# Performance work log

Hardware: AMD Instinct MI355X
Metric: run time of the kernel (lower is better)

Reference implementation:

```python
import jax, jax.numpy as jnp
import numpy as np

D_MODEL = 512
N_HEADS = 8
D_KEYS = D_MODEL // N_HEADS  # 64
DIN = D_MODEL * 2            # 1024
DPROJ = D_KEYS * N_HEADS * 2 # 1024
B, L = 2, 2048


def setup_inputs() -> dict:
    key = jax.random.key(0)
    ks = jax.random.split(key, 11)
    s_in = 1.0 / np.sqrt(DIN)
    s_out = 1.0 / np.sqrt(DPROJ)
    return {
        "queries": jax.random.normal(ks[0], (B, L, DIN), jnp.float32),
        "keys": jax.random.normal(ks[1], (B, L, DIN), jnp.float32),
        "values": jax.random.normal(ks[2], (B, L, DIN), jnp.float32),
        "Wq": jax.random.normal(ks[3], (DPROJ, DIN), jnp.float32) * s_in,
        "bq": jax.random.normal(ks[4], (DPROJ,), jnp.float32) * s_in,
        "Wk": jax.random.normal(ks[5], (DPROJ, DIN), jnp.float32) * s_in,
        "bk": jax.random.normal(ks[6], (DPROJ,), jnp.float32) * s_in,
        "Wv": jax.random.normal(ks[7], (DPROJ, DIN), jnp.float32) * s_in,
        "bv": jax.random.normal(ks[8], (DPROJ,), jnp.float32) * s_in,
        "Wo": jax.random.normal(ks[9], (DIN, DPROJ), jnp.float32) * s_out,
        "bo": jax.random.normal(ks[10], (DIN,), jnp.float32) * s_out,
    }


def reference(queries, keys, values, Wq, bq, Wk, bk, Wv, bv, Wo, bo):
    b, l, _ = queries.shape
    H, E = N_HEADS, 2
    # projections: (B, L, DIN) -> (B, L, d_keys, H, 2)
    q = (queries @ Wq.T + bq).reshape(b, l, -1, H, E)
    k = (keys @ Wk.T + bk).reshape(b, l, -1, H, E)
    v = (values @ Wv.T + bv).reshape(b, l, -1, H, E)
    scale = 1.0 / np.sqrt(E)  # E=2 (real/imag)
    # attention over the d_keys axis, per token n, per head h
    scores = jnp.einsum('bnlhe,bnshe->bnhls', q, k)  # (B, L, H, dk, dk)
    A = jax.nn.softmax(scale * scores, axis=-1)
    out = jnp.einsum('bnhls,bnshd->bnlhd', A, v)     # (B, L, dk, H, 2)
    out = out.reshape(b, l, -1)                      # (B, L, dk*H*2)
    return out @ Wo.T + bo                           # (B, L, 2*d_model)
```

## Files before the change

### kernel.cpp

```cpp
#include <hip/hip_runtime.h>
#include <hip/hip_bf16.h>
#include <stdint.h>

#define TOK   4096
#define KDIM  1024
#define NDIM  1024
#define NHEAD 8

typedef _Float16 f16;
typedef __attribute__((ext_vector_type(2))) _Float16 h2;
typedef __attribute__((ext_vector_type(8))) _Float16 f16x8;
typedef __attribute__((ext_vector_type(4))) float f32x4;
typedef __attribute__((ext_vector_type(4))) uint u32x4;

__device__ __forceinline__ void gload_lds16(const void* g, void* l) {
    __builtin_amdgcn_global_load_lds(
        (const __attribute__((address_space(1))) void*)g,
        (__attribute__((address_space(3))) void*)l, 16, 0, 0);
}


struct CvtArgs {
    const float* src[7];
    void*        dst[7];
    int          n4[7];
    int          type[7];
};

__global__ __launch_bounds__(256) void cvt_kernel(CvtArgs a) {
    const int seg = blockIdx.y;
    const int type = a.type[seg];
    const float4* s = (const float4*)a.src[seg];
    const int n4 = a.n4[seg];
    const int stride = gridDim.x * blockDim.x;
    for (int i = blockIdx.x * blockDim.x + threadIdx.x; i < n4; i += stride) {
        float4 v = s[i];
        if (type == 0) {
            f16* d = (f16*)a.dst[seg];
            union { f16 h[4]; uint2 u; } o;
            o.h[0] = (f16)v.x; o.h[1] = (f16)v.y; o.h[2] = (f16)v.z; o.h[3] = (f16)v.w;
            *(uint2*)(d + (size_t)i * 4) = o.u;
        } else if (type == 1) {
            f16* d = (f16*)a.dst[seg];
            const int r = i >> 8, c = (i & 255) * 4;
            const int rp = ((r >> 1) & 7) * 128 + (r >> 4) * 2 + (r & 1);
            union { f16 h[4]; uint2 u; } o;
            o.h[0] = (f16)v.x; o.h[1] = (f16)v.y; o.h[2] = (f16)v.z; o.h[3] = (f16)v.w;
            *(uint2*)(d + (size_t)rp * 1024 + c) = o.u;
        } else {
            f16* d = (f16*)a.dst[seg];
            const int r = i >> 8, c = (i & 255) * 4;
            const int p0 = ((c >> 1) & 7) * 128 + (c >> 4) * 2;
            const int p1 = (((c + 2) >> 1) & 7) * 128 + ((c + 2) >> 4) * 2;
            union { f16 h[2]; uint u; } u01, u23;
            u01.h[0] = (f16)v.x; u01.h[1] = (f16)v.y;
            u23.h[0] = (f16)v.z; u23.h[1] = (f16)v.w;
            *(uint*)(d + (size_t)r * 1024 + p0) = u01.u;
            *(uint*)(d + (size_t)r * 1024 + p1) = u23.u;
        }
    }
}

struct GemmArgs {
    const f16*   A[3];
    const f16*   B[3];
    const float* bias[3];
    void*        C[3];
};

#define VM_WAIT6 asm volatile("s_waitcnt vmcnt(6)" ::: "memory")
#define VM_WAIT0 asm volatile("s_waitcnt vmcnt(0)" ::: "memory")

template<int OUTMODE>
__global__ __launch_bounds__(256) void gemm_bt_kernel(GemmArgs ga) {
    constexpr int K = KDIM, N = NDIM;
    constexpr int NT = K / 64;
    const f16*   A    = ga.A[blockIdx.z];
    const f16*   B    = ga.B[blockIdx.z];
    const float* bias = ga.bias[blockIdx.z];

    __shared__ f16 sm[2 * (128 * 64 + 64 * 64)];

    const int tid  = threadIdx.x;
    const int wave = tid >> 6, lane = tid & 63;
    const int wm = wave >> 1, wn = wave & 1;
    const int bm = blockIdx.x * 128, bn = blockIdx.y * 64;
    const int lrow = lane & 15, kgrp = lane >> 4;

    f32x4 acc[4][2] = {};

    const int colL = (lane & 7) << 3;
    const int colG = (((lane & 7) ^ ((lane >> 3) & 7)) << 3);
    const int arow = wave * 32 + (lane >> 3);
    const int brow = wave * 16 + (lane >> 3);

    auto stage = [&](int buf, int kt) {
        f16* As = sm + buf * (128 * 64 + 64 * 64);
        f16* Bs = As + 128 * 64;
        #pragma unroll
        for (int i = 0; i < 4; ++i) {
            const int row = arow + i * 8;
            gload_lds16(A + (size_t)(bm + row) * K + kt + colG, As + row * 64 + colL);
        }
        #pragma unroll
        for (int i = 0; i < 2; ++i) {
            const int row = brow + i * 8;
            gload_lds16(B + (size_t)(bn + row) * K + kt + colG, Bs + row * 64 + colL);
        }
    };

    stage(0, 0);

    const int swz = (lrow & 7) << 3;

    for (int it = 0; it < NT; ++it) {
        const int cur = it & 1;
        if (it + 1 < NT) {
            stage(cur ^ 1, (it + 1) * 64);
            VM_WAIT6;
        } else {
            VM_WAIT0;
        }
        __builtin_amdgcn_s_barrier();
        __builtin_amdgcn_sched_barrier(0);

        const f16* As = sm + cur * (128 * 64 + 64 * 64);
        const f16* Bs = As + 128 * 64;
        #pragma unroll
        for (int kk = 0; kk < 2; ++kk) {
            f16x8 af[4], bf[2];
            const int kcol = (kk * 32 + kgrp * 8) ^ swz;
            #pragma unroll
            for (int mi = 0; mi < 4; ++mi)
                af[mi] = *(const f16x8*)(As + (wm * 64 + mi * 16 + lrow) * 64 + kcol);
            #pragma unroll
            for (int ni = 0; ni < 2; ++ni)
                bf[ni] = *(const f16x8*)(Bs + (wn * 32 + ni * 16 + lrow) * 64 + kcol);
            #pragma unroll
            for (int mi = 0; mi < 4; ++mi)
                #pragma unroll
                for (int ni = 0; ni < 2; ++ni)
                    acc[mi][ni] = __builtin_amdgcn_mfma_f32_16x16x32_f16(af[mi], bf[ni], acc[mi][ni], 0, 0, 0);
        }
        __builtin_amdgcn_s_barrier();
    }

    const int rbase = kgrp * 4;
    #pragma unroll
    for (int mi = 0; mi < 4; ++mi) {
        #pragma unroll
        for (int ni = 0; ni < 2; ++ni) {
            const int col = bn + wn * 32 + ni * 16 + lrow;
            const int bidx = (OUTMODE == 0)
                ? (((col >> 1) & 63) * 16 + (col >> 7) * 2 + (col & 1))
                : col;
            const float bv = bias[bidx];
            #pragma unroll
            for (int r = 0; r < 4; ++r) {
                const int row = bm + wm * 64 + mi * 16 + rbase + r;
                const float v = acc[mi][ni][r] + bv;
                if constexpr (OUTMODE == 0)
                    ((f16*)ga.C[blockIdx.z])[(size_t)row * N + col] = (f16)v;
                else
                    ((float*)ga.C[blockIdx.z])[(size_t)row * N + col] = v;
            }
        }
    }
}

__global__ __launch_bounds__(256) void attn_kernel(const f16* qp, const f16* kp,
                                                   const f16* vp, f16* ao) {
    const int tid = threadIdx.x, wave = tid >> 6, lane = tid & 63;
    const int task = blockIdx.x * 4 + wave;
    const size_t base = (size_t)task * 64;
    const float SCALE = 0.70710678118f * 1.44269504089f;

    union U2 { uint u; h2 h; f16 s[2]; };
    U2 qu; qu.u = ((const uint*)qp)[base + lane];
    const float q0 = (float)qu.s[0] * SCALE, q1 = (float)qu.s[1] * SCALE;
#if __has_builtin(__builtin_amdgcn_fdot2)
    h2 qs; qs[0] = (f16)q0; qs[1] = (f16)q1;
#endif

    const u32x4* kb = (const u32x4*)((const uint*)kp + base);
    const u32x4* vb = (const u32x4*)((const uint*)vp + base);

    float sum = 0.f, o0 = 0.f, o1 = 0.f;
    #pragma unroll
    for (int g = 0; g < 4; ++g) {
        u32x4 kr[4], vr[4];
        #pragma unroll
        for (int i = 0; i < 4; ++i) { kr[i] = kb[g * 4 + i]; vr[i] = vb[g * 4 + i]; }
        #pragma unroll
        for (int i = 0; i < 4; ++i) {
            #pragma unroll
            for (int j = 0; j < 4; ++j) {
                U2 ku, vu;
                ku.u = kr[i][j];
                vu.u = vr[i][j];
#if __has_builtin(__builtin_amdgcn_fdot2)
                const float sc = __builtin_amdgcn_fdot2(qs, ku.h, 0.0f, false);
#else
                const float sc = fmaf(q0, (float)ku.s[0], q1 * (float)ku.s[1]);
#endif
#if __has_builtin(__builtin_amdgcn_exp2f)
                const float p = __builtin_amdgcn_exp2f(sc);
#else
                const float p = exp2f(sc);
#endif
                sum += p;
                o0 = fmaf(p, (float)vu.s[0], o0);
                o1 = fmaf(p, (float)vu.s[1], o1);
            }
        }
    }
    const float inv = __builtin_amdgcn_rcpf(sum);
    U2 o;
    o.s[0] = (f16)(o0 * inv);
    o.s[1] = (f16)(o1 * inv);
    ((uint*)ao)[base + lane] = o.u;
}

extern "C" void kernel_launch(void* const* d_in, const int* in_sizes, int n_in,
                              void* d_out, int out_size, void* d_ws, size_t ws_size,
                              hipStream_t stream) {
    const float* queries = (const float*)d_in[0];
    const float* keys    = (const float*)d_in[1];
    const float* values  = (const float*)d_in[2];
    const float* Wq = (const float*)d_in[3];
    const float* bq = (const float*)d_in[4];
    const float* Wk = (const float*)d_in[5];
    const float* bk = (const float*)d_in[6];
    const float* Wv = (const float*)d_in[7];
    const float* bv = (const float*)d_in[8];
    const float* Wo = (const float*)d_in[9];
    const float* bo = (const float*)d_in[10];

    char* ws = (char*)d_ws;
    const size_t MB = 1024 * 1024;
    f16* Xq  = (f16*)(ws + 0 * MB);
    f16* Xk  = (f16*)(ws + 8 * MB);
    f16* Xv  = (f16*)(ws + 16 * MB);
    f16* Wqh = (f16*)(ws + 24 * MB);
    f16* Wkh = (f16*)(ws + 26 * MB);
    f16* Wvh = (f16*)(ws + 28 * MB);
    f16* Woh = (f16*)(ws + 30 * MB);
    f16* qp  = (f16*)(ws + 32 * MB);
    f16* kp  = (f16*)(ws + 40 * MB);
    f16* vp  = (f16*)(ws + 48 * MB);
    f16* ao  = (f16*)(ws + 56 * MB);

    CvtArgs ca;
    ca.src[0] = queries; ca.dst[0] = Xq;  ca.n4[0] = TOK * KDIM / 4;  ca.type[0] = 0;
    ca.src[1] = keys;    ca.dst[1] = Xk;  ca.n4[1] = TOK * KDIM / 4;  ca.type[1] = 0;
    ca.src[2] = values;  ca.dst[2] = Xv;  ca.n4[2] = TOK * KDIM / 4;  ca.type[2] = 0;
    ca.src[3] = Wq;      ca.dst[3] = Wqh; ca.n4[3] = NDIM * KDIM / 4; ca.type[3] = 1;
    ca.src[4] = Wk;      ca.dst[4] = Wkh; ca.n4[4] = NDIM * KDIM / 4; ca.type[4] = 1;
    ca.src[5] = Wv;      ca.dst[5] = Wvh; ca.n4[5] = NDIM * KDIM / 4; ca.type[5] = 1;
    ca.src[6] = Wo;      ca.dst[6] = Woh; ca.n4[6] = NDIM * KDIM / 4; ca.type[6] = 2;
    cvt_kernel<<<dim3(256, 7), 256, 0, stream>>>(ca);

    GemmArgs g1;
    g1.A[0] = Xq;  g1.A[1] = Xk;  g1.A[2] = Xv;
    g1.B[0] = Wqh; g1.B[1] = Wkh; g1.B[2] = Wvh;
    g1.bias[0] = bq; g1.bias[1] = bk; g1.bias[2] = bv;
    g1.C[0] = qp; g1.C[1] = kp; g1.C[2] = vp;
    gemm_bt_kernel<0><<<dim3(32, 16, 3), 256, 0, stream>>>(g1);

    attn_kernel<<<TOK * NHEAD / 4, 256, 0, stream>>>(qp, kp, vp, ao);

    GemmArgs g2;
    g2.A[0] = ao; g2.B[0] = Woh; g2.bias[0] = bo; g2.C[0] = d_out;
    g2.A[1] = ao; g2.B[1] = Woh; g2.bias[1] = bo; g2.C[1] = d_out;
    g2.A[2] = ao; g2.B[2] = Woh; g2.bias[2] = bo; g2.C[2] = d_out;
    gemm_bt_kernel<1><<<dim3(32, 16, 1), 256, 0, stream>>>(g2);
}
```

Before: 193.9 us.

## Stage per-token K/V in LDS and use packed FMA in attention kernel

The attention kernel now assigns one 512-thread block per token (all 8 heads), loading K once coalesced into LDS and V into LDS pre-converted to fp32 pairs. Each wave then reads its head's keys and values from LDS instead of each lane re-reading the same 256 bytes from global memory. The inner loop uses a packed 2-wide FMA for the output accumulation and splits the sum into two accumulators to shorten dependency chains. This adds a block-wide barrier and LDS traffic, and doubles V's storage size in LDS.

```diff
diff --git a/kernel.cpp b/kernel.cpp
--- a/kernel.cpp
+++ b/kernel.cpp
@@ -10,8 +10,15 @@
 typedef _Float16 f16;
 typedef __attribute__((ext_vector_type(2))) _Float16 h2;
 typedef __attribute__((ext_vector_type(8))) _Float16 f16x8;
+typedef __attribute__((ext_vector_type(2))) float f32x2;
 typedef __attribute__((ext_vector_type(4))) float f32x4;
 typedef __attribute__((ext_vector_type(4))) uint u32x4;
+
+#if __has_builtin(__builtin_amdgcn_exp2f)
+#define EXP2(x) __builtin_amdgcn_exp2f(x)
+#else
+#define EXP2(x) exp2f(x)
+#endif
 
 __device__ __forceinline__ void gload_lds16(const void* g, void* l) {
     __builtin_amdgcn_global_load_lds(
@@ -168,57 +175,58 @@
     }
 }
 
-__global__ __launch_bounds__(256) void attn_kernel(const f16* qp, const f16* kp,
+__global__ __launch_bounds__(512) void attn_kernel(const f16* qp, const f16* kp,
                                                    const f16* vp, f16* ao) {
-    const int tid = threadIdx.x, wave = tid >> 6, lane = tid & 63;
-    const int task = blockIdx.x * 4 + wave;
-    const size_t base = (size_t)task * 64;
+    __shared__ __align__(16) uint   kls[512];
+    __shared__ __align__(16) f32x2  vls[512];
+    const int tid = threadIdx.x, head = tid >> 6, lane = tid & 63;
+    const size_t base = (size_t)blockIdx.x * 512;
     const float SCALE = 0.70710678118f * 1.44269504089f;
 
     union U2 { uint u; h2 h; f16 s[2]; };
-    U2 qu; qu.u = ((const uint*)qp)[base + lane];
+    kls[tid] = ((const uint*)kp)[base + tid];
+    U2 vu; vu.u = ((const uint*)vp)[base + tid];
+    vls[tid] = (f32x2){(float)vu.s[0], (float)vu.s[1]};
+
+    U2 qu; qu.u = ((const uint*)qp)[base + tid];
     const float q0 = (float)qu.s[0] * SCALE, q1 = (float)qu.s[1] * SCALE;
 #if __has_builtin(__builtin_amdgcn_fdot2)
     h2 qs; qs[0] = (f16)q0; qs[1] = (f16)q1;
 #endif
-
-    const u32x4* kb = (const u32x4*)((const uint*)kp + base);
-    const u32x4* vb = (const u32x4*)((const uint*)vp + base);
-
-    float sum = 0.f, o0 = 0.f, o1 = 0.f;
+    __syncthreads();
+
+    const u32x4* kb = (const u32x4*)&kls[head * 64];
+    const f32x4* vb = (const f32x4*)&vls[head * 64];
+
+    f32x2 o01 = {0.f, 0.f};
+    float sum0 = 0.f, sum1 = 0.f;
     #pragma unroll
     for (int g = 0; g < 4; ++g) {
-        u32x4 kr[4], vr[4];
-        #pragma unroll
-        for (int i = 0; i < 4; ++i) { kr[i] = kb[g * 4 + i]; vr[i] = vb[g * 4 + i]; }
-        #pragma unroll
-        for (int i = 0; i < 4; ++i) {
-            #pragma unroll
-            for (int j = 0; j < 4; ++j) {
-                U2 ku, vu;
-                ku.u = kr[i][j];
-                vu.u = vr[i][j];
+        u32x4 kr[4];
+        f32x4 vr[8];
+        #pragma unroll
+        for (int i = 0; i < 4; ++i) kr[i] = kb[g * 4 + i];
+        #pragma unroll
+        for (int i = 0; i < 8; ++i) vr[i] = vb[g * 8 + i];
+        #pragma unroll
+        for (int s = 0; s < 16; ++s) {
+            U2 ku; ku.u = kr[s >> 2][s & 3];
 #if __has_builtin(__builtin_amdgcn_fdot2)
-                const float sc = __builtin_amdgcn_fdot2(qs, ku.h, 0.0f, false);
+            const float sc = __builtin_amdgcn_fdot2(qs, ku.h, 0.0f, false);
 #else
-                const float sc = fmaf(q0, (float)ku.s[0], q1 * (float)ku.s[1]);
+            const float sc = fmaf(q0, (float)ku.s[0], q1 * (float)ku.s[1]);
 #endif
-#if __has_builtin(__builtin_amdgcn_exp2f)
-                const float p = __builtin_amdgcn_exp2f(sc);
-#else
-                const float p = exp2f(sc);
-#endif
-                sum += p;
-                o0 = fmaf(p, (float)vu.s[0], o0);
-                o1 = fmaf(p, (float)vu.s[1], o1);
-            }
-        }
-    }
-    const float inv = __builtin_amdgcn_rcpf(sum);
+            const float p = EXP2(sc);
+            if (s & 1) sum1 += p; else sum0 += p;
+            const f32x2 v2 = {vr[s >> 1][(s & 1) << 1], vr[s >> 1][((s & 1) << 1) + 1]};
+            o01 = __builtin_elementwise_fma((f32x2){p, p}, v2, o01);
+        }
+    }
+    const float inv = __builtin_amdgcn_rcpf(sum0 + sum1);
     U2 o;
-    o.s[0] = (f16)(o0 * inv);
-    o.s[1] = (f16)(o1 * inv);
-    ((uint*)ao)[base + lane] = o.u;
+    o.s[0] = (f16)(o01.x * inv);
+    o.s[1] = (f16)(o01.y * inv);
+    ((uint*)ao)[base + tid] = o.u;
 }
 
 extern "C" void kernel_launch(void* const* d_in, const int* in_sizes, int n_in,
@@ -267,7 +275,7 @@
     g1.C[0] = qp; g1.C[1] = kp; g1.C[2] = vp;
     gemm_bt_kernel<0><<<dim3(32, 16, 3), 256, 0, stream>>>(g1);
 
-    attn_kernel<<<TOK * NHEAD / 4, 256, 0, stream>>>(qp, kp, vp, ao);
+    attn_kernel<<<TOK, 512, 0, stream>>>(qp, kp, vp, ao);
 
     GemmArgs g2;
     g2.A[0] = ao; g2.B[0] = Woh; g2.bias[0] = bo; g2.C[0] = d_out;
```

New measurement: 192.6 us. About the same (-0.7%).
